# Optimization experiments

Hardware: AMD Instinct MI355X
Metric: run time of the kernel (lower is better)

## Reference

```python
import jax, jax.numpy as jnp
import numpy as np

ROPE_DIM = 16      # RotaryEmbedding(dim=16)
MAX_FREQ = 256.0   # freqs_for='pixel'
NUM_HEADS = 16


def _axis_freqs(n):
    # pixel mode: base freqs = linspace(1, max_freq/2, dim//2) * pi, pos = linspace(-1, 1, n)
    base = jnp.linspace(1.0, MAX_FREQ / 2.0, ROPE_DIM // 2) * jnp.pi  # (8,)
    pos = jnp.linspace(-1.0, 1.0, n)                                   # (n,)
    f = pos[:, None] * base[None, :]                                   # (n, 8)
    return jnp.repeat(f, 2, axis=-1)                                   # (n, 16) interleaved pairs


def axial_freqs(T, H, W):
    ft = jnp.broadcast_to(_axis_freqs(T)[:, None, None, :], (T, H, W, ROPE_DIM))
    fh = jnp.broadcast_to(_axis_freqs(H)[None, :, None, :], (T, H, W, ROPE_DIM))
    fw = jnp.broadcast_to(_axis_freqs(W)[None, None, :, :], (T, H, W, ROPE_DIM))
    return jnp.concatenate([ft, fh, fw], axis=-1)  # (T, H, W, 48)


def rotate_half(x):
    # interleaved pairs: (..., d*2) -> rotate each (x1, x2) -> (-x2, x1)
    x = x.reshape(*x.shape[:-1], -1, 2)
    x1, x2 = x[..., 0], x[..., 1]
    return jnp.stack([-x2, x1], axis=-1).reshape(*x.shape[:-2], -1)


def apply_rope(freqs, t):
    # freqs: (T, H, W, rot_dim); t: (B, nh, T, H, W, hd); rotate first rot_dim dims
    rd = freqs.shape[-1]
    tm, tr = t[..., :rd], t[..., rd:]
    tm = tm * jnp.cos(freqs) + rotate_half(tm) * jnp.sin(freqs)
    return jnp.concatenate([tm, tr], axis=-1)


def setup_inputs() -> dict:
    key = jax.random.key(0)
    k1, k2, k3, k4 = jax.random.split(key, 4)
    B, N, C = 2, 2048, 1152
    return {
        "x": jax.random.normal(k1, (B, N, C), dtype=jnp.float32),
        "Wqkv": jax.random.normal(k2, (C, 3 * C), dtype=jnp.float32) * 0.02,
        "Wproj": jax.random.normal(k3, (C, C), dtype=jnp.float32) * 0.02,
        "bproj": jax.random.normal(k4, (C,), dtype=jnp.float32) * 0.02,
        "T": 8, "H": 16, "W": 16,
    }


def reference(x, Wqkv, Wproj, bproj, T, H, W):
    B, N, C = x.shape
    nh = NUM_HEADS
    hd = C // nh
    qkv = (x @ Wqkv).reshape(B, N, 3, nh, hd).transpose(2, 0, 3, 1, 4)  # (3, B, nh, N, hd)
    q, k, v = qkv[0], qkv[1], qkv[2]
    # tokens -> video grid
    q = q.reshape(B, nh, T, H, W, hd)
    k = k.reshape(B, nh, T, H, W, hd)
    freqs = axial_freqs(T, H, W)  # (T, H, W, 48)
    q = apply_rope(freqs, q).reshape(B, nh, N, hd)
    k = apply_rope(freqs, k).reshape(B, nh, N, hd)
    # SDPA (no mask, no dropout in eval / kv_cache=None path)
    scale = 1.0 / np.sqrt(hd)
    attn = jax.nn.softmax(jnp.einsum('bhqd,bhkd->bhqk', q, k) * scale, axis=-1)
    o = jnp.einsum('bhqk,bhkd->bhqd', attn, v)  # (B, nh, N, hd)
    o = o.transpose(0, 2, 1, 3).reshape(B, N, C)
    return o @ Wproj + bproj
```

## Files before the change

kernel.cpp:

```cpp
#include <hip/hip_runtime.h>
#include <hip/hip_bf16.h>

#define B_   2
#define N_   2048
#define C_   1152
#define NH   16
#define HD   72
#define HDP  96
#define HDV  80
#define QSTR 3584
#define KROW 104
#define VROW 72
#define KVB  64
#define KCH  832
#define TCH  1552
#define WCH  388

typedef __attribute__((ext_vector_type(8))) short bf16x8;
typedef __attribute__((ext_vector_type(4))) float f32x4;

__device__ __forceinline__ short f2bf(float f) {
  union { float fv; unsigned int u; } v; v.fv = f;
  unsigned int r = v.u + 0x7fffu + ((v.u >> 16) & 1u);
  return (short)(r >> 16);
}

__device__ __forceinline__ float bf2f(short s) {
  union { unsigned u; float f; } v; v.u = ((unsigned)(unsigned short)s) << 16;
  return v.f;
}

__device__ __forceinline__ unsigned pack_bf16(float a, float b) {
  union { __hip_bfloat162 h; unsigned u; } c;
  c.h = __float22bfloat162_rn(make_float2(a, b));
  return c.u;
}

__device__ __forceinline__ void gload_lds16(const short* g, short* l) {
  __builtin_amdgcn_global_load_lds(
      (const __attribute__((address_space(1))) unsigned int*)g,
      (__attribute__((address_space(3))) unsigned int*)l, 16, 0, 0);
}

__global__ __launch_bounds__(256) void prep(
    const float* __restrict__ x, short* __restrict__ xb,
    const float* __restrict__ Wqkv, short* __restrict__ Wt,
    const float* __restrict__ Wproj, short* __restrict__ Wpt,
    float2* __restrict__ trig) {
  int bid = blockIdx.x;
  if (bid < 4608) {
    const int i = bid * 256 + threadIdx.x;
    float4 v = ((const float4*)x)[i];
    short4 s;
    s.x = f2bf(v.x); s.y = f2bf(v.y); s.z = f2bf(v.z); s.w = f2bf(v.w);
    ((short4*)xb)[i] = s;
    return;
  }
  bid -= 4608;
  if (bid >= 4032 + 1296) {
    const int idx = (bid - 4032 - 1296) * 256 + threadIdx.x;
    const int n = idx / 24, p = idx - (idx / 24) * 24;
    const float PI = 3.14159265358979323846f;
    float pos;
    if (p < 8)       pos = -1.f + (2.f / 7.f)  * (float)(n >> 8);
    else if (p < 16) pos = -1.f + (2.f / 15.f) * (float)((n >> 4) & 15);
    else             pos = -1.f + (2.f / 15.f) * (float)(n & 15);
    const float base = (1.f + (127.f / 7.f) * (float)(p & 7)) * PI;
    const float f = pos * base;
    trig[idx] = make_float2(cosf(f), sinf(f));
    return;
  }
  const float* src; short* dst; int Cc, bx, by;
  if (bid < 4032) {
    bx = bid % 112; by = bid / 112; src = Wqkv; dst = Wt; Cc = 3456;
  } else {
    bid -= 4032;
    bx = bid % 36; by = bid / 36; src = Wproj; dst = Wpt; Cc = 1152;
  }
  __shared__ float tile[32][33];
  const int c0 = bx * 32, r0 = by * 32;
  const int tx = threadIdx.x & 31, ty = threadIdx.x >> 5;
  for (int i = ty; i < 32; i += 8)
    tile[i][tx] = (c0 + tx < Cc) ? src[(long)(r0 + i) * Cc + c0 + tx] : 0.f;
  __syncthreads();
  for (int i = ty; i < 32; i += 8)
    dst[(long)(c0 + i) * 1152 + r0 + tx] = f2bf(tile[tx][i]);
}

template<bool BIAS, bool OBF>
__global__ __launch_bounds__(256, 2) void gemm_bt(
    const short* __restrict__ A, const short* __restrict__ Bt,
    void* __restrict__ Cv, const float* __restrict__ bias,
    int M, int N, int K) {
  __shared__ __align__(16) short As[2][128 * 32];
  __shared__ __align__(16) short Bs[2][128 * 32];
  const int t = threadIdx.x;
  const int lane = t & 63, wid = t >> 6;
  const int fr = lane & 15, fq = lane >> 4;

  int lin = blockIdx.y * gridDim.x + blockIdx.x;
  const int q8 = (int)(gridDim.x * gridDim.y) >> 3;
  lin = (lin & 7) * q8 + (lin >> 3);
  const int bm = lin / (int)gridDim.x;
  const int bn = lin - bm * (int)gridDim.x;

  const int wr = (wid >> 1) * 64, wc = (wid & 1) * 64;

  const int srow = t >> 2;
  const int scol = (t & 3) * 8;
  const short* Ag = A + (long)(bm * 128 + srow) * K + scol;
  const short* Bg = Bt + (long)(bn * 128 + srow) * K + scol;

  f32x4 acc[4][4] = {};

  auto STAGE = [&](int kt, int bufi) {
    gload_lds16(Ag + kt * 32,                &As[bufi][t * 8]);
    gload_lds16(Ag + kt * 32 + (long)64 * K, &As[bufi][2048 + t * 8]);
    gload_lds16(Bg + kt * 32,                &Bs[bufi][t * 8]);
    gload_lds16(Bg + kt * 32 + (long)64 * K, &Bs[bufi][2048 + t * 8]);
  };

  const int NKT = K / 32;
  STAGE(0, 0);

  for (int kt = 0; kt < NKT; ++kt) {
    const int cur = kt & 1;
    if (kt + 1 < NKT) {
      STAGE(kt + 1, cur ^ 1);
      asm volatile("s_waitcnt vmcnt(4)" ::: "memory");
    } else {
      asm volatile("s_waitcnt vmcnt(0)" ::: "memory");
    }
    __builtin_amdgcn_s_barrier();

    bf16x8 af[4], bf[4];
    #pragma unroll
    for (int i = 0; i < 4; ++i)
      af[i] = *(const bf16x8*)(&As[cur][(wr + i * 16 + fr) * 32 + fq * 8]);
    #pragma unroll
    for (int j = 0; j < 4; ++j)
      bf[j] = *(const bf16x8*)(&Bs[cur][(wc + j * 16 + fr) * 32 + fq * 8]);
    __builtin_amdgcn_s_setprio(1);
    #pragma unroll
    for (int i = 0; i < 4; ++i)
      #pragma unroll
      for (int j = 0; j < 4; ++j)
        acc[i][j] = __builtin_amdgcn_mfma_f32_16x16x32_bf16(af[i], bf[j], acc[i][j], 0, 0, 0);
    __builtin_amdgcn_s_setprio(0);
    __builtin_amdgcn_s_barrier();
  }

  #pragma unroll
  for (int i = 0; i < 4; ++i) {
    #pragma unroll
    for (int j = 0; j < 4; ++j) {
      const long row0 = (long)bm * 128 + wr + i * 16 + fq * 4;
      const int col = bn * 128 + wc + j * 16 + fr;
      const float bv = BIAS ? bias[col] : 0.f;
      #pragma unroll
      for (int r = 0; r < 4; ++r) {
        const float val = acc[i][j][r] + bv;
        if constexpr (OBF)
          ((short*)Cv)[(row0 + r) * (long)N + col] = f2bf(val);
        else
          ((float*)Cv)[(row0 + r) * (long)N + col] = val;
      }
    }
  }
}

__global__ __launch_bounds__(512, 2) void gemm_bt256(
    const short* __restrict__ A, const short* __restrict__ Bt,
    short* __restrict__ Cv, int M, int N, int K) {
  __shared__ __align__(16) short As[2][256 * 64];
  __shared__ __align__(16) short Bs[2][256 * 64];
  const int t = threadIdx.x;
  const int lane = t & 63, wid = t >> 6;
  const int fr = lane & 15, fq = lane >> 4;
  const int wm = wid >> 2, wn = wid & 3;
  const int rx = fr & 7;

  int lin = blockIdx.y * gridDim.x + blockIdx.x;
  const int q8 = (int)(gridDim.x * gridDim.y) >> 3;
  lin = (lin & 7) * q8 + (lin >> 3);
  const int bm = lin / (int)gridDim.x;
  const int bn = lin - bm * (int)gridDim.x;

  int soff[4];
  #pragma unroll
  for (int r = 0; r < 4; ++r) {
    const int p = r * 512 + t;
    const int row = p >> 3, pc = p & 7;
    soff[r] = row * K + (pc ^ (row & 7)) * 8;
  }
  const short* Ag = A + (long)bm * 256 * K;
  const short* Bg = Bt + (long)bn * 256 * K;

  f32x4 acc[8][4] = {};

  const int NKT = K / 64;
  #pragma unroll
  for (int r = 0; r < 4; ++r)
    gload_lds16(Ag + soff[r], &As[0][(r * 512 + t) * 8]);
  #pragma unroll
  for (int r = 0; r < 4; ++r)
    gload_lds16(Bg + soff[r], &Bs[0][(r * 512 + t) * 8]);

  for (int kt = 0; kt < NKT; ++kt) {
    const int cur = kt & 1;
    const bool pre = (kt + 1 < NKT);
    asm volatile("s_waitcnt vmcnt(0)" ::: "memory");
    __builtin_amdgcn_s_barrier();
    const short* Ac = &As[cur][0];
    const short* Bc = &Bs[cur][0];
    bf16x8 af[4][2], bf0[2][2], bf1[2][2];

    if (pre) {
      #pragma unroll
      for (int r = 0; r < 4; ++r)
        gload_lds16(Ag + soff[r] + (kt + 1) * 64, &As[cur ^ 1][(r * 512 + t) * 8]);
    }
    #pragma unroll
    for (int i = 0; i < 4; ++i)
      #pragma unroll
      for (int kk = 0; kk < 2; ++kk)
        af[i][kk] = *(const bf16x8*)(Ac + (wm * 128 + i * 16 + fr) * 64 + (((kk * 4 + fq) ^ rx) * 8));
    #pragma unroll
    for (int j = 0; j < 2; ++j)
      #pragma unroll
      for (int kk = 0; kk < 2; ++kk)
        bf0[j][kk] = *(const bf16x8*)(Bc + (wn * 64 + j * 16 + fr) * 64 + (((kk * 4 + fq) ^ rx) * 8));
    __builtin_amdgcn_s_setprio(1);
    #pragma unroll
    for (int i = 0; i < 4; ++i)
      #pragma unroll
      for (int j = 0; j < 2; ++j)
        #pragma unroll
        for (int kk = 0; kk < 2; ++kk)
          acc[i][j] = __builtin_amdgcn_mfma_f32_16x16x32_bf16(af[i][kk], bf0[j][kk], acc[i][j], 0, 0, 0);
    __builtin_amdgcn_s_setprio(0);

    if (pre) {
      #pragma unroll
      for (int r = 0; r < 4; ++r)
        gload_lds16(Bg + soff[r] + (kt + 1) * 64, &Bs[cur ^ 1][(r * 512 + t) * 8]);
    }
    #pragma unroll
    for (int j = 0; j < 2; ++j)
      #pragma unroll
      for (int kk = 0; kk < 2; ++kk)
        bf1[j][kk] = *(const bf16x8*)(Bc + (wn * 64 + 32 + j * 16 + fr) * 64 + (((kk * 4 + fq) ^ rx) * 8));
    __builtin_amdgcn_s_setprio(1);
    #pragma unroll
    for (int i = 0; i < 4; ++i)
      #pragma unroll
      for (int j = 0; j < 2; ++j)
        #pragma unroll
        for (int kk = 0; kk < 2; ++kk)
          acc[i][2 + j] = __builtin_amdgcn_mfma_f32_16x16x32_bf16(af[i][kk], bf1[j][kk], acc[i][2 + j], 0, 0, 0);
    __builtin_amdgcn_s_setprio(0);

    #pragma unroll
    for (int i = 0; i < 4; ++i)
      #pragma unroll
      for (int kk = 0; kk < 2; ++kk)
        af[i][kk] = *(const bf16x8*)(Ac + (wm * 128 + 64 + i * 16 + fr) * 64 + (((kk * 4 + fq) ^ rx) * 8));
    __builtin_amdgcn_s_setprio(1);
    #pragma unroll
    for (int i = 0; i < 4; ++i)
      #pragma unroll
      for (int j = 0; j < 2; ++j)
        #pragma unroll
        for (int kk = 0; kk < 2; ++kk)
          acc[4 + i][j] = __builtin_amdgcn_mfma_f32_16x16x32_bf16(af[i][kk], bf0[j][kk], acc[4 + i][j], 0, 0, 0);
    __builtin_amdgcn_s_setprio(0);

    __builtin_amdgcn_s_setprio(1);
    #pragma unroll
    for (int i = 0; i < 4; ++i)
      #pragma unroll
      for (int j = 0; j < 2; ++j)
        #pragma unroll
        for (int kk = 0; kk < 2; ++kk)
          acc[4 + i][2 + j] = __builtin_amdgcn_mfma_f32_16x16x32_bf16(af[i][kk], bf1[j][kk], acc[4 + i][2 + j], 0, 0, 0);
    __builtin_amdgcn_s_setprio(0);
  }

  #pragma unroll
  for (int mi = 0; mi < 8; ++mi) {
    #pragma unroll
    for (int j = 0; j < 4; ++j) {
      const long row0 = (long)bm * 256 + wm * 128 + (mi >> 2) * 64 + (mi & 3) * 16 + fq * 4;
      const int col = bn * 256 + wn * 64 + j * 16 + fr;
      #pragma unroll
      for (int r = 0; r < 4; ++r)
        Cv[(row0 + r) * (long)N + col] = f2bf(acc[mi][j][r]);
    }
  }
}

__global__ __launch_bounds__(256) void rope_pack(
    const short* __restrict__ QKV, const float2* __restrict__ trig,
    short* __restrict__ Kp, short* __restrict__ Vt) {
  const int blk = blockIdx.x;
  const int nt = blk & 15;
  const int h = (blk >> 4) & 15;
  const int b = blk >> 8;
  const int t = threadIdx.x;
  const int n0 = nt * 128;
  const long bhn = ((long)(b * NH + h)) * N_;

  for (int idx = t; idx < 128 * 48; idx += 256) {
    const int r = idx / 48;
    const int p = idx - r * 48;
    const int n = n0 + r;
    float vx = 0.f, vy = 0.f;
    if (p < 36) {
      short2 v2 = *(const short2*)(QKV + ((long)(b * N_ + n)) * QSTR + C_ + h * HD + 2 * p);
      vx = bf2f(v2.x); vy = bf2f(v2.y);
    }
    float o0 = vx, o1 = vy;
    if (p < 24) {
      const float2 cs = trig[n * 24 + p];
      o0 = vx * cs.x - vy * cs.y;
      o1 = vy * cs.x + vx * cs.y;
    }
    short2 ov; ov.x = f2bf(o0); ov.y = f2bf(o1);
    *(short2*)(Kp + (bhn + n) * HDP + 2 * p) = ov;
  }

  __shared__ short vt[128][82];
  for (int idx = t; idx < 128 * 40; idx += 256) {
    const int r = idx / 40, p = idx - r * 40;
    short2 v2; v2.x = 0; v2.y = 0;
    if (p < 36)
      v2 = *(const short2*)(QKV + ((long)(b * N_ + n0 + r)) * QSTR + 2 * C_ + h * HD + 2 * p);
    *(short2*)(&vt[r][2 * p]) = v2;
  }
  __syncthreads();
  for (int idx = t; idx < HDV * 128; idx += 256) {
    const int d = idx >> 7, nn = idx & 127;
    const int c = nn & 31;
    const int nsrc = (nn & 96) | (((c >> 2) & 1) * 16 + ((c >> 3) & 3) * 4 + (c & 3));
    Vt[(((long)(b * NH + h)) * HDV + d) * N_ + n0 + nn] = vt[nsrc][d];
  }
}

#define QKT_STEP(BUFI, S)                                                      \
  {                                                                            \
    const short* KsC_ = &KV[(BUFI)][0];                                        \
    __builtin_amdgcn_s_setprio(1);                                             \
    _Pragma("unroll")                                                          \
    for (int j = 0; j < 4; ++j) {                                              \
      _Pragma("unroll")                                                        \
      for (int kk = 0; kk < 3; ++kk) {                                         \
        bf16x8 kf = *(const bf16x8*)(KsC_ + (j * 16 + fr) * KROW + (kk * 4 + fq) * 8); \
        S[0][j] = __builtin_amdgcn_mfma_f32_16x16x32_bf16(kf, qf[0][kk], S[0][j], 0, 0, 0); \
        S[1][j] = __builtin_amdgcn_mfma_f32_16x16x32_bf16(kf, qf[1][kk], S[1][j], 0, 0, 0); \
      }                                                                        \
    }                                                                          \
    __builtin_amdgcn_s_setprio(0);                                             \
  }

#define ATTN_STEP(T, SCUR, SNEXT)                                              \
  {                                                                            \
    const int t_ = (T);                                                        \
    _Pragma("unroll")                                                          \
    for (int i = 0; i < 2; ++i) {                                              \
      float psum = 0.f;                                                        \
      _Pragma("unroll")                                                        \
      for (int j = 0; j < 4; ++j)                                              \
        _Pragma("unroll")                                                      \
        for (int r = 0; r < 4; ++r) {                                          \
          const float p = __builtin_amdgcn_exp2f(SCUR[i][j][r]);               \
          SCUR[i][j][r] = p;                                                   \
          psum += p;                                                           \
        }                                                                      \
      l_[i] += psum;                                                           \
    }                                                                          \
    asm volatile("s_waitcnt vmcnt(0)" ::: "memory");                           \
    __builtin_amdgcn_s_barrier();                                              \
    if (t_ + 2 < 32) STAGE(t_ + 2, (t_ + 2) % 3);                              \
    if (t_ + 1 < 32) {                                                         \
      _Pragma("unroll")                                                        \
      for (int i = 0; i < 2; ++i)                                              \
        _Pragma("unroll")                                                      \
        for (int j = 0; j < 4; ++j)                                            \
          SNEXT[i][j] = (f32x4){0.f, 0.f, 0.f, 0.f};                           \
      QKT_STEP((t_ + 1) % 3, SNEXT);                                           \
    }                                                                          \
    const short* VsC_ = &KV[t_ % 3][KCH * 8];                                  \
    __builtin_amdgcn_s_setprio(1);                                             \
    _Pragma("unroll")                                                          \
    for (int g = 0; g < 2; ++g) {                                              \
      union { unsigned u[4]; bf16x8 v; } pf0, pf1;                             \
      pf0.u[0] = pack_bf16(SCUR[0][2 * g][0],     SCUR[0][2 * g][1]);          \
      pf0.u[1] = pack_bf16(SCUR[0][2 * g][2],     SCUR[0][2 * g][3]);          \
      pf0.u[2] = pack_bf16(SCUR[0][2 * g + 1][0], SCUR[0][2 * g + 1][1]);      \
      pf0.u[3] = pack_bf16(SCUR[0][2 * g + 1][2], SCUR[0][2 * g + 1][3]);      \
      pf1.u[0] = pack_bf16(SCUR[1][2 * g][0],     SCUR[1][2 * g][1]);          \
      pf1.u[1] = pack_bf16(SCUR[1][2 * g][2],     SCUR[1][2 * g][3]);          \
      pf1.u[2] = pack_bf16(SCUR[1][2 * g + 1][0], SCUR[1][2 * g + 1][1]);      \
      pf1.u[3] = pack_bf16(SCUR[1][2 * g + 1][2], SCUR[1][2 * g + 1][3]);      \
      _Pragma("unroll")                                                        \
      for (int jd = 0; jd < 5; ++jd) {                                         \
        bf16x8 vf = *(const bf16x8*)(VsC_ + (jd * 16 + fr) * VROW + (g * 4 + fq) * 8); \
        accO[0][jd] = __builtin_amdgcn_mfma_f32_16x16x32_bf16(pf0.v, vf, accO[0][jd], 0, 0, 0); \
        accO[1][jd] = __builtin_amdgcn_mfma_f32_16x16x32_bf16(pf1.v, vf, accO[1][jd], 0, 0, 0); \
      }                                                                        \
    }                                                                          \
    __builtin_amdgcn_s_setprio(0);                                             \
  }

__global__ __launch_bounds__(256, 2) void attn(
    const short* __restrict__ QKVb, const short* __restrict__ Kp,
    const short* __restrict__ Vt, const float2* __restrict__ trig,
    short* __restrict__ Aproj) {
  __shared__ __align__(16) short KV[3][TCH * 8];
  int blk = blockIdx.x;
  blk = (blk & 7) * 64 + (blk >> 3);
  const int qt = blk & 15;
  const int h = (blk >> 4) & 15;
  const int b = blk >> 8;
  const int t = threadIdx.x, lane = t & 63, wid = t >> 6;
  const int fr = lane & 15, fq = lane >> 4;

  const long bh = (long)(b * NH + h);
  const short* Kg = Kp + bh * N_ * HDP;
  const short* Vg = Vt + bh * HDV * N_;

  const short* sb[7];
  int sstr[7];
  #pragma unroll
  for (int it = 0; it < 7; ++it) {
    int g = wid * WCH + (it < 6 ? it * 64 + lane : 384 + lane);
    if (g >= TCH) g = TCH - 1;
    if (g < KCH) {
      const int r = g / 13, c = g - r * 13;
      sb[it] = Kg + r * HDP + (c < 12 ? c * 8 : 0);
      sstr[it] = KVB * HDP;
    } else {
      const int v = g - KCH;
      const int r = v / 9, c = v - r * 9;
      sb[it] = Vg + r * N_ + (c < 8 ? c * 8 : 0);
      sstr[it] = KVB;
    }
  }

  f32x4 accO[2][5] = {};
  float l_[2] = {0.f, 0.f};

  auto STAGE = [&](int kt, int bufi) {
    short* D = &KV[bufi][0];
    #pragma unroll
    for (int it = 0; it < 6; ++it)
      gload_lds16(sb[it] + kt * sstr[it], D + (wid * WCH + it * 64 + lane) * 8);
    if (lane < 4)
      gload_lds16(sb[6] + kt * sstr[6], D + (wid * WCH + 384 + lane) * 8);
  };

  {
    short* QD = &KV[2][0];
    #pragma unroll
    for (int it = 0; it < 5; ++it) {
      const int g = wid * 288 + (it < 4 ? it * 64 + lane : 256 + (lane & 31));
      const int r = g / 9, c = g - r * 9;
      const short* src = QKVb + ((long)(b * N_ + qt * 128 + r)) * QSTR + h * HD + (c < 8 ? c * 8 : 64);
      if (it < 4 || lane < 32)
        gload_lds16(src, QD + g * 8);
    }
  }
  STAGE(0, 0);
  STAGE(1, 1);
  asm volatile("s_waitcnt vmcnt(14)" ::: "memory");
  __builtin_amdgcn_s_barrier();

  const float qscale = 0.17002324f;
  bf16x8 qf[2][3];
  {
    const short* Qlds = &KV[2][0];
    #pragma unroll
    for (int i = 0; i < 2; ++i) {
      const int n = qt * 128 + wid * 32 + i * 16 + fr;
      const int lrow = wid * 32 + i * 16 + fr;
      #pragma unroll
      for (int kk = 0; kk < 3; ++kk) {
        const int col = kk * 32 + fq * 8;
        union { short s[8]; bf16x8 v; } raw;
        if (col < HD)
          raw.v = *(const bf16x8*)(Qlds + lrow * 72 + col);
        else
          #pragma unroll
          for (int z = 0; z < 8; ++z) raw.s[z] = 0;
        union { short s[8]; bf16x8 v; } outv;
        #pragma unroll
        for (int e = 0; e < 4; ++e) {
          const int p = kk * 16 + fq * 4 + e;
          const float vx = bf2f(raw.s[2 * e]), vy = bf2f(raw.s[2 * e + 1]);
          float o0 = vx, o1 = vy;
          if (p < 24) {
            const float2 cs = trig[n * 24 + p];
            o0 = vx * cs.x - vy * cs.y;
            o1 = vy * cs.x + vx * cs.y;
          }
          outv.s[2 * e]     = f2bf(o0 * qscale);
          outv.s[2 * e + 1] = f2bf(o1 * qscale);
        }
        qf[i][kk] = outv.v;
      }
    }
  }

  asm volatile("s_waitcnt vmcnt(7)" ::: "memory");
  __builtin_amdgcn_s_barrier();

  f32x4 sA[2][4], sB[2][4];
  #pragma unroll
  for (int i = 0; i < 2; ++i)
    #pragma unroll
    for (int j = 0; j < 4; ++j)
      sA[i][j] = (f32x4){0.f, 0.f, 0.f, 0.f};
  QKT_STEP(0, sA);

  for (int kt2 = 0; kt2 < 16; ++kt2) {
    ATTN_STEP(2 * kt2,     sA, sB);
    ATTN_STEP(2 * kt2 + 1, sB, sA);
  }

  #pragma unroll
  for (int i = 0; i < 2; ++i) {
    l_[i] += __shfl_xor(l_[i], 16);
    l_[i] += __shfl_xor(l_[i], 32);
  }
  float linv[2] = {1.f / l_[0], 1.f / l_[1]};
  #pragma unroll
  for (int i = 0; i < 2; ++i) {
    float li[4];
    #pragma unroll
    for (int r = 0; r < 4; ++r) li[r] = __shfl(linv[i], fq * 4 + r);
    #pragma unroll
    for (int r = 0; r < 4; ++r) {
      const long n = qt * 128 + wid * 32 + i * 16 + fq * 4 + r;
      #pragma unroll
      for (int jd = 0; jd < 5; ++jd) {
        const int d = jd * 16 + fr;
        if (d < HD)
          Aproj[((long)b * N_ + n) * C_ + h * HD + d] = f2bf(accO[i][jd][r] * li[r]);
      }
    }
  }
}

extern "C" void kernel_launch(void* const* d_in, const int* in_sizes, int n_in,
                              void* d_out, int out_size, void* d_ws, size_t ws_size,
                              hipStream_t stream) {
  const float* x     = (const float*)d_in[0];
  const float* Wqkv  = (const float*)d_in[1];
  const float* Wproj = (const float*)d_in[2];
  const float* bproj = (const float*)d_in[3];
  float* out = (float*)d_out;

  char* ws = (char*)d_ws;
  short* QKVb = (short*)ws;         size_t off = (size_t)4096 * QSTR * 2;
  short* xb  = (short*)(ws + off);  off += (size_t)4096 * 1152 * 2;
  short* Wt  = (short*)(ws + off);  off += (size_t)QSTR * 1152 * 2;
  short* Wpt = (short*)(ws + off);  off += (size_t)1152 * 1152 * 2;
  short* Kp  = (short*)(ws + off);  off += (size_t)B_ * NH * N_ * HDP * 2;
  short* Vt  = (short*)(ws + off);  off += (size_t)B_ * NH * HDV * N_ * 2;
  short* Ap  = (short*)(ws + off);  off += (size_t)4096 * 1152 * 2;
  float2* trig = (float2*)(ws + off);  off += (size_t)N_ * 24 * 8;

  prep<<<4608 + 4032 + 1296 + 192, 256, 0, stream>>>(x, xb, Wqkv, Wt, Wproj, Wpt, trig);
  gemm_bt256<<<dim3(QSTR / 256, 4096 / 256), 512, 0, stream>>>(
      xb, Wt, QKVb, 4096, QSTR, 1152);
  rope_pack<<<B_ * NH * (N_ / 128), 256, 0, stream>>>(QKVb, trig, Kp, Vt);
  attn<<<B_ * NH * (N_ / 128), 256, 0, stream>>>(QKVb, Kp, Vt, trig, Ap);
  gemm_bt<true, false><<<dim3(1152 / 128, 4096 / 128), 256, 0, stream>>>(
      Ap, Wpt, (void*)out, bproj, 4096, 1152, 1152);
}
```

Before: 167.7 us.

## Fuse K rotary embedding into QKV GEMM epilogue, shrink pack kernel to V

The QKV GEMM epilogue now applies RoPE to K columns directly from fp32 accumulators, using a lane shuffle to get the pair partner, and writes K straight into the padded per-head Kp layout. The separate rope_pack kernel becomes vpack, which only zero-fills the K padding and transposes V. This removes a bf16 round-trip read of K and a pass over the K data. In exchange the GEMM epilogue gets branchy, scattered 2-byte stores with a trig lookup. Rotating from fp32 values also changes rounding slightly.

Result: slower. 176.0 us (+5.0%).

```diff
diff --git a/kernel.cpp b/kernel.cpp
--- a/kernel.cpp
+++ b/kernel.cpp
@@ -171,7 +171,8 @@
 
 __global__ __launch_bounds__(512, 2) void gemm_bt256(
     const short* __restrict__ A, const short* __restrict__ Bt,
-    short* __restrict__ Cv, int M, int N, int K) {
+    short* __restrict__ Cv, short* __restrict__ Kp,
+    const float2* __restrict__ trig, int M, int N, int K) {
   __shared__ __align__(16) short As[2][256 * 64];
   __shared__ __align__(16) short Bs[2][256 * 64];
   const int t = threadIdx.x;
@@ -292,16 +293,35 @@
     for (int j = 0; j < 4; ++j) {
       const long row0 = (long)bm * 256 + wm * 128 + (mi >> 2) * 64 + (mi & 3) * 16 + fq * 4;
       const int col = bn * 256 + wn * 64 + j * 16 + fr;
-      #pragma unroll
-      for (int r = 0; r < 4; ++r)
-        Cv[(row0 + r) * (long)N + col] = f2bf(acc[mi][j][r]);
-    }
-  }
-}
-
-__global__ __launch_bounds__(256) void rope_pack(
-    const short* __restrict__ QKV, const float2* __restrict__ trig,
-    short* __restrict__ Kp, short* __restrict__ Vt) {
+      if (col >= C_ && col < 2 * C_) {
+        const int cr = col - C_;
+        const int h = cr / HD;
+        const int d = cr - h * HD;
+        #pragma unroll
+        for (int r = 0; r < 4; ++r) {
+          const float v = acc[mi][j][r];
+          const float pv = __shfl_xor(v, 1);
+          float o = v;
+          if (d < 48) {
+            const int n = (int)((row0 + r) & (N_ - 1));
+            const float2 cs = trig[n * 24 + (d >> 1)];
+            o = (d & 1) ? (v * cs.x + pv * cs.y) : (v * cs.x - pv * cs.y);
+          }
+          const long bb = (row0 + r) >> 11;
+          const long n  = (row0 + r) & (N_ - 1);
+          Kp[((bb * NH + h) * N_ + n) * HDP + d] = f2bf(o);
+        }
+      } else {
+        #pragma unroll
+        for (int r = 0; r < 4; ++r)
+          Cv[(row0 + r) * (long)N + col] = f2bf(acc[mi][j][r]);
+      }
+    }
+  }
+}
+
+__global__ __launch_bounds__(256) void vpack(
+    const short* __restrict__ QKV, short* __restrict__ Kp, short* __restrict__ Vt) {
   const int blk = blockIdx.x;
   const int nt = blk & 15;
   const int h = (blk >> 4) & 15;
@@ -310,28 +330,14 @@
   const int n0 = nt * 128;
   const long bhn = ((long)(b * NH + h)) * N_;
 
-  for (int idx = t; idx < 128 * 48; idx += 256) {
-    const int r = idx / 48;
-    const int p = idx - r * 48;
-    const int n = n0 + r;
-    float vx = 0.f, vy = 0.f;
-    if (p < 36) {
-      short2 v2 = *(const short2*)(QKV + ((long)(b * N_ + n)) * QSTR + C_ + h * HD + 2 * p);
-      vx = bf2f(v2.x); vy = bf2f(v2.y);
-    }
-    float o0 = vx, o1 = vy;
-    if (p < 24) {
-      const float2 cs = trig[n * 24 + p];
-      o0 = vx * cs.x - vy * cs.y;
-      o1 = vy * cs.x + vx * cs.y;
-    }
-    short2 ov; ov.x = f2bf(o0); ov.y = f2bf(o1);
-    *(short2*)(Kp + (bhn + n) * HDP + 2 * p) = ov;
+  for (int idx = t; idx < 128 * 24; idx += 256) {
+    const int r = idx / 24, d = HD + (idx - (idx / 24) * 24);
+    Kp[(bhn + n0 + r) * HDP + d] = 0;
   }
 
   __shared__ short vt[128][82];
   for (int idx = t; idx < 128 * 40; idx += 256) {
-    const int r = idx / 40, p = idx - r * 40;
+    const int r = idx / 40, p = idx - (idx / 40) * 40;
     short2 v2; v2.x = 0; v2.y = 0;
     if (p < 36)
       v2 = *(const short2*)(QKV + ((long)(b * N_ + n0 + r)) * QSTR + 2 * C_ + h * HD + 2 * p);
@@ -572,8 +578,8 @@
 
   prep<<<4608 + 4032 + 1296 + 192, 256, 0, stream>>>(x, xb, Wqkv, Wt, Wproj, Wpt, trig);
   gemm_bt256<<<dim3(QSTR / 256, 4096 / 256), 512, 0, stream>>>(
-      xb, Wt, QKVb, 4096, QSTR, 1152);
-  rope_pack<<<B_ * NH * (N_ / 128), 256, 0, stream>>>(QKVb, trig, Kp, Vt);
+      xb, Wt, QKVb, Kp, trig, 4096, QSTR, 1152);
+  vpack<<<B_ * NH * (N_ / 128), 256, 0, stream>>>(QKVb, Kp, Vt);
   attn<<<B_ * NH * (N_ / 128), 256, 0, stream>>>(QKVb, Kp, Vt, trig, Ap);
   gemm_bt<true, false><<<dim3(1152 / 128, 4096 / 128), 256, 0, stream>>>(
       Ap, Wpt, (void*)out, bproj, 4096, 1152, 1152);
```
